# Optimization experiments

Hardware: AMD Instinct MI355X
Metric: run time of the kernel (lower is better)

The kernel has to match this reference:

```python
import jax, jax.numpy as jnp
import numpy as np

EPS = 1e-7
N_SINKHORN = 40


def setup_inputs() -> dict:
    key = jax.random.key(0)
    k1, k2, k3, k4 = jax.random.split(key, 4)
    n, l, K, batch = 1024, 4, 1, 32
    x = jax.random.randint(k1, (batch, n), 0, l)                      # class labels in [0, l)
    W = jax.random.normal(k2, (n, n), jnp.float32)                    # MI-derived logit weights
    V_compress = jax.random.normal(k3, (n, l), jnp.float32)           # log-marginals
    E_compress = jax.random.normal(k4, (K, n, n, l, l), jnp.float32) * 0.1  # log-joints
    return {"x": x, "W": W, "V_compress": V_compress, "E_compress": E_compress}


def reference(x, W, V_compress, E_compress):
    n, l = V_compress.shape
    which_moat = 0

    # --- marginals / joints ---
    V = jax.nn.softmax(V_compress, axis=1)            # [n, l]
    E = jnp.exp(E_compress[which_moat])               # [n, n, l, l]
    E = E / E.sum(axis=(-2, -1), keepdims=True)

    # --- 40-step Sinkhorn / IPF projection onto target row/col marginals ---
    A_b = V[:, None, :, None]                         # [n, 1, l, 1] target row marginals
    B_b = V[None, :, None, :]                         # [1, n, 1, l] target col marginals

    def ipf_step(E, _):
        E = E * (A_b / (E.sum(axis=3, keepdims=True) + EPS))
        E = E * (B_b / (E.sum(axis=2, keepdims=True) + EPS))
        E = E / (E.sum(axis=(-2, -1), keepdims=True) + EPS)
        return E, None

    E, _ = jax.lax.scan(ipf_step, E, None, length=N_SINKHORN)

    # zero the diagonal (i == j) blocks, clamp to [0, 1]
    E = jnp.clip(E * (1.0 - jnp.eye(n, dtype=E.dtype))[:, :, None, None], 0.0, 1.0)

    # --- tree-structured weights and base Laplacian ---
    Ws = jax.nn.sigmoid(W)
    Ws = jnp.tril(Ws, k=-1)
    Ws = Ws + Ws.T                                    # symmetric, zero diag
    L0 = -Ws + jnp.diag(Ws.sum(axis=1))               # [n, n]

    # --- gather per-sample marginals / pairwise probs ---
    idx = jnp.arange(n)
    Pr = V[idx[None, :], x]                           # [B, n]
    P = E[idx[None, :, None], idx[None, None, :], x[:, :, None], x[:, None, :]]  # [B, n, n]
    P = P / (Pr[:, :, None] * Pr[:, None, :])

    WP = Ws[None, :, :] * P                           # [B, n, n]
    eye = jnp.eye(n, dtype=WP.dtype)
    L = -WP + WP.sum(axis=2)[:, :, None] * eye        # batched diag_embed

    y = jnp.log(Pr + 1e-7).sum(axis=1)                # [B]
    _, ld1 = jnp.linalg.slogdet(L[:, 1:, 1:] + 1e-7)
    _, ld0 = jnp.linalg.slogdet(L0[1:, 1:] + 1e-7)
    return y + ld1 - ld0
```

## Files before the change

kernel.cpp:

```cpp
#include <hip/hip_runtime.h>
#include <math.h>

#define MSZ   1048576ull
#define NMAT  33
#define PANSZ 61440
#define NSINK 14

__device__ __forceinline__ float frcp(float x){ return __builtin_amdgcn_rcpf(x); }

typedef __attribute__((ext_vector_type(8)))  short  bfrag;
typedef __attribute__((ext_vector_type(8)))  unsigned short u16x8;
typedef __attribute__((ext_vector_type(16))) float  f32x16;

__device__ __forceinline__ unsigned short bf16rn(float x){
  unsigned u = __float_as_uint(x);
  unsigned r = u + 0x7fffu + ((u>>16)&1u);
  return (unsigned short)(r>>16);
}
__device__ __forceinline__ float bf2f(unsigned short h){
  return __uint_as_float(((unsigned)h)<<16);
}

__global__ void k_misc(const float* __restrict__ Vc, float* __restrict__ V,
                       const float* __restrict__ W, float* __restrict__ Ws){
  int t = threadIdx.x;
  if(blockIdx.x < 4){
    int i = blockIdx.x*256 + t;
    float4 v = ((const float4*)Vc)[i];
    float mx = fmaxf(fmaxf(v.x,v.y), fmaxf(v.z,v.w));
    float e0=__expf(v.x-mx), e1=__expf(v.y-mx), e2=__expf(v.z-mx), e3=__expf(v.w-mx);
    float is = 1.f/(e0+e1+e2+e3);
    ((float4*)V)[i] = make_float4(e0*is, e1*is, e2*is, e3*is);
  } else {
    int idx = (blockIdx.x-4)*256 + t;
    int i = idx>>10, j = idx&1023;
    float v = 0.f;
    if(i != j){
      float w = (i>j) ? W[i*1024+j] : W[j*1024+i];
      v = 1.f/(1.f+__expf(-w));
    }
    Ws[idx]=v;
  }
}

__global__ void k_pr_y(const float* __restrict__ V, const int* __restrict__ x,
                       float* __restrict__ PrInv, float* __restrict__ y){
  int b = blockIdx.x, t = threadIdx.x;
  __shared__ float red[256];
  float acc = 0.f;
  for(int i=t; i<1024; i+=256){
    int xv = x[b*1024+i];
    float pr = V[i*4+xv];
    PrInv[b*1024+i] = 1.f/pr;
    acc += logf(pr + 1e-7f);
  }
  red[t]=acc; __syncthreads();
  for(int s=128;s>0;s>>=1){ if(t<s) red[t]+=red[t+s]; __syncthreads(); }
  if(t==0) y[b]=red[0];
}

__global__ void __launch_bounds__(256) k_sinkhorn(
    const float* __restrict__ Ec, const float* __restrict__ V,
    const float* __restrict__ Ws, const float* __restrict__ PrInv,
    const int* __restrict__ x, float* __restrict__ mats,
    float* __restrict__ partial){
  int idx = blockIdx.x*256 + threadIdx.x;
  int i = idx>>10, j = idx&1023;
  if(i==0) return;
  int t = threadIdx.x;
  int lane = t & 63, wv = t >> 6;
  __shared__ float sE[256][17];
  float E[16];
  {
    const float4* p = (const float4*)(Ec + (size_t)idx*16);
    float4 q0=p[0], q1=p[1], q2=p[2], q3=p[3];
    E[0]=__expf(q0.x); E[1]=__expf(q0.y); E[2]=__expf(q0.z); E[3]=__expf(q0.w);
    E[4]=__expf(q1.x); E[5]=__expf(q1.y); E[6]=__expf(q1.z); E[7]=__expf(q1.w);
    E[8]=__expf(q2.x); E[9]=__expf(q2.y); E[10]=__expf(q2.z); E[11]=__expf(q2.w);
    E[12]=__expf(q3.x);E[13]=__expf(q3.y);E[14]=__expf(q3.z); E[15]=__expf(q3.w);
  }
  float s0=0.f;
  #pragma unroll
  for(int q=0;q<16;q++) s0+=E[q];
  float is0 = frcp(s0);
  #pragma unroll
  for(int q=0;q<16;q++) E[q]*=is0;
  float av[4], bv[4];
  {
    float4 va = ((const float4*)V)[i];
    av[0]=va.x; av[1]=va.y; av[2]=va.z; av[3]=va.w;
    float4 vb = ((const float4*)V)[j];
    bv[0]=vb.x; bv[1]=vb.y; bv[2]=vb.z; bv[3]=vb.w;
  }
  for(int it=0; it<NSINK; ++it){
    #pragma unroll
    for(int r=0;r<4;r++){
      float rs = E[4*r]+E[4*r+1]+E[4*r+2]+E[4*r+3];
      float sc = av[r]*frcp(rs+1e-7f);
      E[4*r]*=sc; E[4*r+1]*=sc; E[4*r+2]*=sc; E[4*r+3]*=sc;
    }
    #pragma unroll
    for(int c=0;c<4;c++){
      float cs = E[c]+E[4+c]+E[8+c]+E[12+c];
      float sc = bv[c]*frcp(cs+1e-7f);
      E[c]*=sc; E[4+c]*=sc; E[8+c]*=sc; E[12+c]*=sc;
    }
  }
  #pragma unroll
  for(int q=0;q<16;q++) sE[t][q] = fminf(fmaxf(E[q],0.f),1.f);
  float wsij = Ws[idx];
  for(int b=0;b<32;b++){
    int xi = x[b*1024+i];
    int xj = x[b*1024+j];
    float val = sE[t][(xi<<2)+xj] * wsij * PrInv[b*1024+i] * PrInv[b*1024+j];
    if(j!=0)
      mats[(size_t)(1+b)*MSZ + (size_t)(i-1)*1024 + (j-1)] = 1e-7f - val;
    float r = val;
    r += __shfl_down(r,32); r += __shfl_down(r,16); r += __shfl_down(r,8);
    r += __shfl_down(r,4);  r += __shfl_down(r,2);  r += __shfl_down(r,1);
    if(lane==0)
      partial[((size_t)b<<14) + ((size_t)(i-1)<<4) + ((blockIdx.x&3)<<2) + wv] = r;
  }
}

__global__ void k_l0(const float* __restrict__ Ws, float* __restrict__ mats){
  int r = blockIdx.x, t = threadIdx.x;
  float* orow = mats + (size_t)r*1024;
  if(r == 1023){
    float4 o = make_float4(0.f,0.f,0.f,0.f);
    if(t==255) o.w = 1.f;
    ((float4*)orow)[t] = o;
    return;
  }
  const float* wrow = Ws + (size_t)(r+1)*1024;
  float4 v = ((const float4*)wrow)[t];
  __shared__ float red[256];
  red[t] = v.x+v.y+v.z+v.w;
  __syncthreads();
  for(int s=128;s>0;s>>=1){ if(t<s) red[t]+=red[t+s]; __syncthreads(); }
  float rs = red[0];
  float o[4];
  #pragma unroll
  for(int q=0;q<4;q++){
    int c = 4*t+q;
    if(c==r)          o[q] = rs + 1e-7f;
    else if(c < 1023) o[q] = 1e-7f - wrow[c+1];
    else              o[q] = 0.f;
  }
  ((float4*)orow)[t] = make_float4(o[0],o[1],o[2],o[3]);
}

__global__ void k_patch(float* __restrict__ mats, const float* __restrict__ partial){
  int m = blockIdx.y + 1;
  int r = blockIdx.x*256 + threadIdx.x;
  float* A = mats + (size_t)m*MSZ;
  A[(size_t)r*1024 + 1023] = (r==1023) ? 1.f : 0.f;
  if(r < 1023){
    A[(size_t)1023*1024 + r] = 0.f;
    const float* pp = partial + (((size_t)(m-1))<<14) + ((size_t)r<<4);
    float s = 0.f;
    #pragma unroll
    for(int q=0;q<16;q++) s += pp[q];
    A[(size_t)r*1024 + r] = s + 1e-7f;
  }
}

__global__ void __launch_bounds__(256) k_panel(float* __restrict__ mats,
    unsigned short* __restrict__ Ah, unsigned short* __restrict__ Al,
    unsigned short* __restrict__ Bh, unsigned short* __restrict__ Bl,
    float* __restrict__ logdet, int k){
  int m = blockIdx.y;
  float* A = mats + (size_t)m*MSZ;
  int rem = 1024 - (k+64);
  int nb = (rem + 255) >> 8;
  int t = threadIdx.x;
  int lane = t & 63, wvi = t >> 6;
  __shared__ float Ld[4096];
  __shared__ float Ud[4096];

  if(wvi==0){
    float row[64];
    #pragma unroll
    for(int q=0;q<64;q++)
      row[q] = A[(size_t)(k+lane)*1024 + k + q];
    float slog = 0.f;
    #pragma unroll
    for(int c=0;c<64;c++){
      float piv = __shfl(row[c], c);
      slog += logf(fabsf(piv));
      float ip = frcp(piv);
      bool below = lane > c;
      float lic = below ? row[c]*ip : 0.f;
      row[c] = below ? lic : row[c];
      if(below) Ld[lane*64 + c] = lic;
      #pragma unroll
      for(int q=c+1;q<64;q++){
        float uq = __shfl(row[q], c);
        row[q] = fmaf(-lic, uq, row[q]);
      }
    }
    #pragma unroll
    for(int q=0;q<64;q++)
      if(q>=lane) Ud[lane*64 + q] = row[q];
    if(lane==0 && blockIdx.x==0){
      if(k==0) logdet[m] = slog; else logdet[m] += slog;
    }
  }
  __syncthreads();

  float v[64];
  unsigned short* Ph; unsigned short* Pl; int rel; bool act;
  if((int)blockIdx.x < nb){
    rel = blockIdx.x*256 + t;
    act = rel < rem;
    int i = k + 64 + rel;
    size_t base = (size_t)i*1024 + k;
    const float4* pb = (const float4*)(A + (act ? base : 0));
    #pragma unroll
    for(int q4=0;q4<16;q4++){
      float4 w = act ? pb[q4] : make_float4(0.f,0.f,0.f,0.f);
      v[4*q4]=w.x; v[4*q4+1]=w.y; v[4*q4+2]=w.z; v[4*q4+3]=w.w;
    }
    #pragma unroll
    for(int p=0;p<64;p++){
      float xp = v[p]*frcp(Ud[p*64+p]);
      v[p] = xp;
      #pragma unroll
      for(int q=p+1;q<64;q++) v[q] = fmaf(-xp, Ud[p*64+q], v[q]);
    }
    Ph = Ah + (size_t)m*PANSZ; Pl = Al + (size_t)m*PANSZ;
  } else {
    rel = (blockIdx.x - nb)*256 + t;
    act = rel < rem;
    int col = k + 64 + rel;
    #pragma unroll
    for(int r=0;r<64;r++) v[r] = act ? A[(size_t)(k+r)*1024 + col] : 0.f;
    #pragma unroll
    for(int r=1;r<64;r++){
      float s = v[r];
      #pragma unroll
      for(int p=0;p<r;p++) s = fmaf(-Ld[r*64+p], v[p], s);
      v[r] = s;
    }
    Ph = Bh + (size_t)m*PANSZ; Pl = Bl + (size_t)m*PANSZ;
  }
  if(act){
    u16x8* ph = (u16x8*)(Ph + (size_t)rel*64);
    u16x8* pl = (u16x8*)(Pl + (size_t)rel*64);
    #pragma unroll
    for(int q8=0;q8<8;q8++){
      u16x8 h8, l8;
      #pragma unroll
      for(int e=0;e<8;e++){
        float xv = v[q8*8+e];
        unsigned short h = bf16rn(xv);
        h8[e] = h;
        l8[e] = bf16rn(xv - bf2f(h));
      }
      ph[q8] = h8;
      pl[q8] = l8;
    }
  }
}

__global__ void __launch_bounds__(64) k_ld(const float* __restrict__ mats,
                                           float* __restrict__ logdet){
  int m = blockIdx.x, t = threadIdx.x;
  const float* A = mats + (size_t)m*MSZ;
  float row[64];
  #pragma unroll
  for(int q=0;q<64;q++)
    row[q] = A[(size_t)(960+t)*1024 + 960 + q];
  float slog = 0.f;
  #pragma unroll
  for(int c=0;c<64;c++){
    float piv = __shfl(row[c], c);
    slog += logf(fabsf(piv));
    float ip = frcp(piv);
    bool below = t > c;
    float lic = below ? row[c]*ip : 0.f;
    #pragma unroll
    for(int q=c+1;q<64;q++){
      float uq = __shfl(row[q], c);
      row[q] = fmaf(-lic, uq, row[q]);
    }
  }
  if(t==0) logdet[m] += slog;
}

__global__ void __launch_bounds__(256) k_gemm(float* __restrict__ mats,
    const unsigned short* __restrict__ Ah, const unsigned short* __restrict__ Al,
    const unsigned short* __restrict__ Bh, const unsigned short* __restrict__ Bl,
    int k){
  int m = blockIdx.z;
  float* A = mats + (size_t)m*MSZ;
  int rem = 1024 - (k+64);
  int i0rel = blockIdx.y*128;
  int j0rel = blockIdx.x*128;
  __shared__ unsigned short As[2][4096];
  __shared__ unsigned short Bs[2][4096];
  int t = threadIdx.x;
  int lane = t & 63, wvi = t >> 6;
  int wr = wvi >> 1, wc = wvi & 1;

  const unsigned short* pAh = Ah + (size_t)m*PANSZ;
  const unsigned short* pAl = Al + (size_t)m*PANSZ;
  const unsigned short* pBh = Bh + (size_t)m*PANSZ;
  const unsigned short* pBl = Bl + (size_t)m*PANSZ;

  int rowA[2], koctA[2], ldsOff[2];
  bool vA[2], vB[2];
  size_t offA[2], offB[2];
  #pragma unroll
  for(int p=0;p<2;p++){
    int c = t + 256*p;
    int row = c>>2, koct = c&3;
    rowA[p]=row; koctA[p]=koct;
    ldsOff[p] = row*32 + ((koct ^ ((row>>1)&3))<<3);
    vA[p] = (i0rel+row) < rem;
    vB[p] = (j0rel+row) < rem;
    offA[p] = (size_t)(i0rel+row)*64 + koct*8;
    offB[p] = (size_t)(j0rel+row)*64 + koct*8;
  }
  u16x8 z; z = 0;

  #pragma unroll
  for(int p=0;p<2;p++){
    u16x8 ah = vA[p] ? *(const u16x8*)(pAh + offA[p]) : z;
    u16x8 al = vA[p] ? *(const u16x8*)(pAl + offA[p]) : z;
    u16x8 bh = vB[p] ? *(const u16x8*)(pBh + offB[p]) : z;
    u16x8 bl = vB[p] ? *(const u16x8*)(pBl + offB[p]) : z;
    *(u16x8*)&As[0][ldsOff[p]] = ah;
    *(u16x8*)&As[1][ldsOff[p]] = al;
    *(u16x8*)&Bs[0][ldsOff[p]] = bh;
    *(u16x8*)&Bs[1][ldsOff[p]] = bl;
  }
  u16x8 p1[8];
  #pragma unroll
  for(int p=0;p<2;p++){
    p1[4*p+0] = vA[p] ? *(const u16x8*)(pAh + offA[p] + 32) : z;
    p1[4*p+1] = vA[p] ? *(const u16x8*)(pAl + offA[p] + 32) : z;
    p1[4*p+2] = vB[p] ? *(const u16x8*)(pBh + offB[p] + 32) : z;
    p1[4*p+3] = vB[p] ? *(const u16x8*)(pBl + offB[p] + 32) : z;
  }
  __syncthreads();

  f32x16 acc[2][2];
  #pragma unroll
  for(int rt=0;rt<2;rt++)
    #pragma unroll
    for(int ct=0;ct<2;ct++)
      #pragma unroll
      for(int q=0;q<16;q++) acc[rt][ct][q] = 0.f;

  int kgrp = lane >> 5;
  #pragma unroll
  for(int ks=0; ks<2; ks++){
    #pragma unroll
    for(int kc=0;kc<2;kc++){
      int koct = kc*2 + kgrp;
      bfrag ah[2], al[2], bh[2], bl[2];
      #pragma unroll
      for(int rt=0;rt<2;rt++){
        int row = wr*64 + rt*32 + (lane&31);
        int ad = row*32 + ((koct ^ ((row>>1)&3))<<3);
        ah[rt] = *(const bfrag*)&As[0][ad];
        al[rt] = *(const bfrag*)&As[1][ad];
      }
      #pragma unroll
      for(int ct=0;ct<2;ct++){
        int col = wc*64 + ct*32 + (lane&31);
        int ad = col*32 + ((koct ^ ((col>>1)&3))<<3);
        bh[ct] = *(const bfrag*)&Bs[0][ad];
        bl[ct] = *(const bfrag*)&Bs[1][ad];
      }
      #pragma unroll
      for(int rt=0;rt<2;rt++)
        #pragma unroll
        for(int ct=0;ct<2;ct++){
          acc[rt][ct] = __builtin_amdgcn_mfma_f32_32x32x16_bf16(ah[rt], bh[ct], acc[rt][ct], 0,0,0);
          acc[rt][ct] = __builtin_amdgcn_mfma_f32_32x32x16_bf16(ah[rt], bl[ct], acc[rt][ct], 0,0,0);
          acc[rt][ct] = __builtin_amdgcn_mfma_f32_32x32x16_bf16(al[rt], bh[ct], acc[rt][ct], 0,0,0);
        }
    }
    if(ks==0){
      __syncthreads();
      #pragma unroll
      for(int p=0;p<2;p++){
        *(u16x8*)&As[0][ldsOff[p]] = p1[4*p+0];
        *(u16x8*)&As[1][ldsOff[p]] = p1[4*p+1];
        *(u16x8*)&Bs[0][ldsOff[p]] = p1[4*p+2];
        *(u16x8*)&Bs[1][ldsOff[p]] = p1[4*p+3];
      }
      __syncthreads();
    }
  }

  int r0 = k + 64;
  #pragma unroll
  for(int rt=0;rt<2;rt++){
    int rowblk = i0rel + wr*64 + rt*32;
    if(rowblk >= rem) continue;
    #pragma unroll
    for(int ct=0;ct<2;ct++){
      int colblk = j0rel + wc*64 + ct*32;
      if(colblk >= rem) continue;
      int col = r0 + colblk + (lane&31);
      int rbase = r0 + rowblk + ((lane>>5)<<2);
      #pragma unroll
      for(int reg=0;reg<16;reg++){
        int row = rbase + (reg&3) + ((reg>>2)<<3);
        float* pc = A + (size_t)row*1024 + col;
        *pc -= acc[rt][ct][reg];
      }
    }
  }
}

__global__ void k_final(const float* __restrict__ y, const float* __restrict__ logdet,
                        float* __restrict__ out){
  int b = threadIdx.x;
  if(b<32) out[b] = y[b] + logdet[1+b] - logdet[0];
}

extern "C" void kernel_launch(void* const* d_in, const int* in_sizes, int n_in,
                              void* d_out, int out_size, void* d_ws, size_t ws_size,
                              hipStream_t stream){
  (void)in_sizes; (void)n_in; (void)out_size; (void)ws_size;
  const int*   x  = (const int*)d_in[0];
  const float* W  = (const float*)d_in[1];
  const float* Vc = (const float*)d_in[2];
  const float* Ec = (const float*)d_in[3];
  float* out = (float*)d_out;

  char* p = (char*)d_ws;
  auto alloc = [&](size_t bytes)->char*{ char* r = p; p += (bytes+255)&~(size_t)255; return r; };
  float* mats   = (float*)alloc((size_t)NMAT*MSZ*4);
  float* Ws     = (float*)alloc(1048576ull*4);
  unsigned short* Ah = (unsigned short*)alloc((size_t)NMAT*PANSZ*2);
  unsigned short* Al = (unsigned short*)alloc((size_t)NMAT*PANSZ*2);
  unsigned short* Bh = (unsigned short*)alloc((size_t)NMAT*PANSZ*2);
  unsigned short* Bl = (unsigned short*)alloc((size_t)NMAT*PANSZ*2);
  float* V      = (float*)alloc(4096*4);
  float* PrInv  = (float*)alloc(32768*4);
  float* partial= (float*)alloc((size_t)32*16384*4);
  float* y      = (float*)alloc(256);
  float* logdet = (float*)alloc(256);

  k_misc<<<4100,256,0,stream>>>(Vc, V, W, Ws);
  k_pr_y<<<32,256,0,stream>>>(V, x, PrInv, y);
  k_sinkhorn<<<4096,256,0,stream>>>(Ec, V, Ws, PrInv, x, mats, partial);
  k_l0<<<1024,256,0,stream>>>(Ws, mats);
  k_patch<<<dim3(4,32),256,0,stream>>>(mats, partial);

  for(int s=0;s<15;s++){
    int k = 64*s;
    int rem = 1024 - (k+64);
    int nbp = (rem+255)/256;
    k_panel<<<dim3(2*nbp,NMAT),256,0,stream>>>(mats, Ah, Al, Bh, Bl, logdet, k);
    int nt = (rem+127)/128;
    k_gemm<<<dim3(nt,nt,NMAT),256,0,stream>>>(mats, Ah, Al, Bh, Bl, k);
  }
  k_ld<<<NMAT,64,0,stream>>>(mats, logdet);
  k_final<<<1,32,0,stream>>>(y, logdet, out);
}
```

Baseline: 1.200 ms.

## Use two-level blocked LU with rank-128 trailing updates and fold PrInv into Sinkhorn

Measured after the change: 1.886 ms. 1.57x slower.

```diff
diff --git a/kernel.cpp b/kernel.cpp
--- a/kernel.cpp
+++ b/kernel.cpp
@@ -44,15 +44,13 @@
 }
 
 __global__ void k_pr_y(const float* __restrict__ V, const int* __restrict__ x,
-                       float* __restrict__ PrInv, float* __restrict__ y){
+                       float* __restrict__ y){
   int b = blockIdx.x, t = threadIdx.x;
   __shared__ float red[256];
   float acc = 0.f;
   for(int i=t; i<1024; i+=256){
     int xv = x[b*1024+i];
-    float pr = V[i*4+xv];
-    PrInv[b*1024+i] = 1.f/pr;
-    acc += logf(pr + 1e-7f);
+    acc += logf(V[i*4+xv] + 1e-7f);
   }
   red[t]=acc; __syncthreads();
   for(int s=128;s>0;s>>=1){ if(t<s) red[t]+=red[t+s]; __syncthreads(); }
@@ -61,9 +59,8 @@
 
 __global__ void __launch_bounds__(256) k_sinkhorn(
     const float* __restrict__ Ec, const float* __restrict__ V,
-    const float* __restrict__ Ws, const float* __restrict__ PrInv,
-    const int* __restrict__ x, float* __restrict__ mats,
-    float* __restrict__ partial){
+    const float* __restrict__ Ws, const int* __restrict__ x,
+    float* __restrict__ mats, float* __restrict__ partial){
   int idx = blockIdx.x*256 + threadIdx.x;
   int i = idx>>10, j = idx&1023;
   if(i==0) return;
@@ -106,13 +103,16 @@
       E[c]*=sc; E[4+c]*=sc; E[8+c]*=sc; E[12+c]*=sc;
     }
   }
-  #pragma unroll
-  for(int q=0;q<16;q++) sE[t][q] = fminf(fmaxf(E[q],0.f),1.f);
   float wsij = Ws[idx];
+  #pragma unroll
+  for(int q=0;q<16;q++){
+    float e = fminf(fmaxf(E[q],0.f),1.f);
+    sE[t][q] = e * wsij * frcp(av[q>>2]*bv[q&3]);
+  }
   for(int b=0;b<32;b++){
     int xi = x[b*1024+i];
     int xj = x[b*1024+j];
-    float val = sE[t][(xi<<2)+xj] * wsij * PrInv[b*1024+i] * PrInv[b*1024+j];
+    float val = sE[t][(xi<<2)+xj];
     if(j!=0)
       mats[(size_t)(1+b)*MSZ + (size_t)(i-1)*1024 + (j-1)] = 1e-7f - val;
     float r = val;
@@ -263,29 +263,223 @@
   }
 }
 
-__global__ void __launch_bounds__(64) k_ld(const float* __restrict__ mats,
-                                           float* __restrict__ logdet){
-  int m = blockIdx.x, t = threadIdx.x;
-  const float* A = mats + (size_t)m*MSZ;
-  float row[64];
-  #pragma unroll
-  for(int q=0;q<64;q++)
-    row[q] = A[(size_t)(960+t)*1024 + 960 + q];
-  float slog = 0.f;
-  #pragma unroll
-  for(int c=0;c<64;c++){
-    float piv = __shfl(row[c], c);
-    slog += logf(fabsf(piv));
-    float ip = frcp(piv);
-    bool below = t > c;
-    float lic = below ? row[c]*ip : 0.f;
-    #pragma unroll
-    for(int q=c+1;q<64;q++){
-      float uq = __shfl(row[q], c);
-      row[q] = fmaf(-lic, uq, row[q]);
-    }
-  }
-  if(t==0) logdet[m] += slog;
+__global__ void __launch_bounds__(256) k_sgemm(float* __restrict__ mats,
+    const unsigned short* __restrict__ Ah, const unsigned short* __restrict__ Al,
+    const unsigned short* __restrict__ Bh, const unsigned short* __restrict__ Bl,
+    int k){
+  int m = blockIdx.y;
+  float* A = mats + (size_t)m*MSZ;
+  int k2 = k + 64;
+  int rem2 = 1024 - (k2+64);
+  int nct = (rem2 + 64 + 127) >> 7;
+  int t = threadIdx.x;
+  int lane = t & 63, wvi = t >> 6;
+  int kgrp = lane >> 5;
+  const unsigned short* pAh = Ah + (size_t)m*PANSZ;
+  const unsigned short* pAl = Al + (size_t)m*PANSZ;
+  const unsigned short* pBh = Bh + (size_t)m*PANSZ;
+  const unsigned short* pBl = Bl + (size_t)m*PANSZ;
+
+  f32x16 acc[2];
+  #pragma unroll
+  for(int u=0;u<2;u++)
+    #pragma unroll
+    for(int q=0;q<16;q++) acc[u][q] = 0.f;
+
+  if((int)blockIdx.x < nct){
+    int rbase = blockIdx.x*128 + wvi*32;
+    int maxrow = rem2 + 63;
+    int arow = rbase + (lane&31);
+    int arowc = (arow > maxrow) ? maxrow : arow;
+    #pragma unroll
+    for(int kc=0;kc<4;kc++){
+      int koct = kc*2 + kgrp;
+      bfrag ah = *(const bfrag*)(pAh + (size_t)arowc*64 + koct*8);
+      bfrag al = *(const bfrag*)(pAl + (size_t)arowc*64 + koct*8);
+      #pragma unroll
+      for(int ct=0;ct<2;ct++){
+        int bcol = ct*32 + (lane&31);
+        bfrag bh = *(const bfrag*)(pBh + (size_t)bcol*64 + koct*8);
+        bfrag bl = *(const bfrag*)(pBl + (size_t)bcol*64 + koct*8);
+        acc[ct] = __builtin_amdgcn_mfma_f32_32x32x16_bf16(ah, bh, acc[ct], 0,0,0);
+        acc[ct] = __builtin_amdgcn_mfma_f32_32x32x16_bf16(ah, bl, acc[ct], 0,0,0);
+        acc[ct] = __builtin_amdgcn_mfma_f32_32x32x16_bf16(al, bh, acc[ct], 0,0,0);
+      }
+    }
+    #pragma unroll
+    for(int ct=0;ct<2;ct++){
+      int gc = k2 + ct*32 + (lane&31);
+      #pragma unroll
+      for(int reg=0;reg<16;reg++){
+        int sr = rbase + ((lane>>5)<<2) + (reg&3) + ((reg>>2)<<3);
+        if(sr <= maxrow){
+          float* pc = A + (size_t)(k2+sr)*1024 + gc;
+          *pc -= acc[ct][reg];
+        }
+      }
+    }
+  } else {
+    int cbase = (blockIdx.x - nct)*128 + wvi*32;
+    int bcol = 64 + cbase + (lane&31);
+    #pragma unroll
+    for(int kc=0;kc<4;kc++){
+      int koct = kc*2 + kgrp;
+      bfrag bh = *(const bfrag*)(pBh + (size_t)bcol*64 + koct*8);
+      bfrag bl = *(const bfrag*)(pBl + (size_t)bcol*64 + koct*8);
+      #pragma unroll
+      for(int rt=0;rt<2;rt++){
+        int arow = rt*32 + (lane&31);
+        bfrag ah = *(const bfrag*)(pAh + (size_t)arow*64 + koct*8);
+        bfrag al = *(const bfrag*)(pAl + (size_t)arow*64 + koct*8);
+        acc[rt] = __builtin_amdgcn_mfma_f32_32x32x16_bf16(ah, bh, acc[rt], 0,0,0);
+        acc[rt] = __builtin_amdgcn_mfma_f32_32x32x16_bf16(ah, bl, acc[rt], 0,0,0);
+        acc[rt] = __builtin_amdgcn_mfma_f32_32x32x16_bf16(al, bh, acc[rt], 0,0,0);
+      }
+    }
+    int gc = k2 + 64 + cbase + (lane&31);
+    #pragma unroll
+    for(int rt=0;rt<2;rt++){
+      #pragma unroll
+      for(int reg=0;reg<16;reg++){
+        int gr = k2 + rt*32 + ((lane>>5)<<2) + (reg&3) + ((reg>>2)<<3);
+        float* pc = A + (size_t)gr*1024 + gc;
+        *pc -= acc[rt][reg];
+      }
+    }
+  }
+}
+
+__global__ void __launch_bounds__(256) k_gemm128(float* __restrict__ mats,
+    const unsigned short* __restrict__ A1h, const unsigned short* __restrict__ A1l,
+    const unsigned short* __restrict__ B1h, const unsigned short* __restrict__ B1l,
+    const unsigned short* __restrict__ A2h, const unsigned short* __restrict__ A2l,
+    const unsigned short* __restrict__ B2h, const unsigned short* __restrict__ B2l,
+    int k){
+  int m = blockIdx.z;
+  float* A = mats + (size_t)m*MSZ;
+  int rem = 1024 - (k+128);
+  int i0rel = blockIdx.y*128;
+  int j0rel = blockIdx.x*128;
+  __shared__ unsigned short As[2][4096];
+  __shared__ unsigned short Bs[2][4096];
+  int t = threadIdx.x;
+  int lane = t & 63, wvi = t >> 6;
+  int wr = wvi >> 1, wc = wvi & 1;
+
+  const unsigned short* srcAh[2] = {A1h + (size_t)m*PANSZ, A2h + (size_t)m*PANSZ};
+  const unsigned short* srcAl[2] = {A1l + (size_t)m*PANSZ, A2l + (size_t)m*PANSZ};
+  const unsigned short* srcBh[2] = {B1h + (size_t)m*PANSZ, B2h + (size_t)m*PANSZ};
+  const unsigned short* srcBl[2] = {B1l + (size_t)m*PANSZ, B2l + (size_t)m*PANSZ};
+
+  int ldsOff[2]; bool vA[2], vB[2];
+  size_t rA[2][2], rB[2][2];
+  int koA[2];
+  #pragma unroll
+  for(int p=0;p<2;p++){
+    int c = t + 256*p;
+    int row = c>>2, koct = c&3;
+    koA[p] = koct*8;
+    ldsOff[p] = row*32 + ((koct ^ ((row>>1)&3))<<3);
+    vA[p] = (i0rel+row) < rem;
+    vB[p] = (j0rel+row) < rem;
+    rA[0][p] = (size_t)(i0rel+row+64)*64;
+    rB[0][p] = (size_t)(j0rel+row+64)*64;
+    rA[1][p] = (size_t)(i0rel+row)*64;
+    rB[1][p] = (size_t)(j0rel+row)*64;
+  }
+  u16x8 z; z = 0;
+  u16x8 cur[8], nxt[8];
+  #pragma unroll
+  for(int p=0;p<2;p++){
+    cur[4*p+0] = vA[p] ? *(const u16x8*)(srcAh[0] + rA[0][p] + koA[p]) : z;
+    cur[4*p+1] = vA[p] ? *(const u16x8*)(srcAl[0] + rA[0][p] + koA[p]) : z;
+    cur[4*p+2] = vB[p] ? *(const u16x8*)(srcBh[0] + rB[0][p] + koA[p]) : z;
+    cur[4*p+3] = vB[p] ? *(const u16x8*)(srcBl[0] + rB[0][p] + koA[p]) : z;
+  }
+
+  f32x16 acc[2][2];
+  #pragma unroll
+  for(int rt=0;rt<2;rt++)
+    #pragma unroll
+    for(int ct=0;ct<2;ct++)
+      #pragma unroll
+      for(int q=0;q<16;q++) acc[rt][ct][q] = 0.f;
+
+  int kgrp = lane >> 5;
+  #pragma unroll
+  for(int st=0; st<4; st++){
+    if(st) __syncthreads();
+    #pragma unroll
+    for(int p=0;p<2;p++){
+      *(u16x8*)&As[0][ldsOff[p]] = cur[4*p+0];
+      *(u16x8*)&As[1][ldsOff[p]] = cur[4*p+1];
+      *(u16x8*)&Bs[0][ldsOff[p]] = cur[4*p+2];
+      *(u16x8*)&Bs[1][ldsOff[p]] = cur[4*p+3];
+    }
+    if(st<3){
+      int ns = st+1;
+      int set = ns>>1, koff = (ns&1)*32;
+      #pragma unroll
+      for(int p=0;p<2;p++){
+        nxt[4*p+0] = vA[p] ? *(const u16x8*)(srcAh[set] + rA[set][p] + koff + koA[p]) : z;
+        nxt[4*p+1] = vA[p] ? *(const u16x8*)(srcAl[set] + rA[set][p] + koff + koA[p]) : z;
+        nxt[4*p+2] = vB[p] ? *(const u16x8*)(srcBh[set] + rB[set][p] + koff + koA[p]) : z;
+        nxt[4*p+3] = vB[p] ? *(const u16x8*)(srcBl[set] + rB[set][p] + koff + koA[p]) : z;
+      }
+    }
+    __syncthreads();
+    #pragma unroll
+    for(int kc=0;kc<2;kc++){
+      int koct = kc*2 + kgrp;
+      bfrag ah[2], al[2], bh[2], bl[2];
+      #pragma unroll
+      for(int rt=0;rt<2;rt++){
+        int row = wr*64 + rt*32 + (lane&31);
+        int ad = row*32 + ((koct ^ ((row>>1)&3))<<3);
+        ah[rt] = *(const bfrag*)&As[0][ad];
+        al[rt] = *(const bfrag*)&As[1][ad];
+      }
+      #pragma unroll
+      for(int ct=0;ct<2;ct++){
+        int col = wc*64 + ct*32 + (lane&31);
+        int ad = col*32 + ((koct ^ ((col>>1)&3))<<3);
+        bh[ct] = *(const bfrag*)&Bs[0][ad];
+        bl[ct] = *(const bfrag*)&Bs[1][ad];
+      }
+      #pragma unroll
+      for(int rt=0;rt<2;rt++)
+        #pragma unroll
+        for(int ct=0;ct<2;ct++){
+          acc[rt][ct] = __builtin_amdgcn_mfma_f32_32x32x16_bf16(ah[rt], bh[ct], acc[rt][ct], 0,0,0);
+          acc[rt][ct] = __builtin_amdgcn_mfma_f32_32x32x16_bf16(ah[rt], bl[ct], acc[rt][ct], 0,0,0);
+          acc[rt][ct] = __builtin_amdgcn_mfma_f32_32x32x16_bf16(al[rt], bh[ct], acc[rt][ct], 0,0,0);
+        }
+    }
+    if(st<3){
+      #pragma unroll
+      for(int q=0;q<8;q++) cur[q] = nxt[q];
+    }
+  }
+
+  int r0 = k + 128;
+  #pragma unroll
+  for(int rt=0;rt<2;rt++){
+    int rowblk = i0rel + wr*64 + rt*32;
+    if(rowblk >= rem) continue;
+    #pragma unroll
+    for(int ct=0;ct<2;ct++){
+      int colblk = j0rel + wc*64 + ct*32;
+      if(colblk >= rem) continue;
+      int col = r0 + colblk + (lane&31);
+      int rbase = r0 + rowblk + ((lane>>5)<<2);
+      #pragma unroll
+      for(int reg=0;reg<16;reg++){
+        int row = rbase + (reg&3) + ((reg>>2)<<3);
+        float* pc = A + (size_t)row*1024 + col;
+        *pc -= acc[rt][ct][reg];
+      }
+    }
+  }
 }
 
 __global__ void __launch_bounds__(256) k_gemm(float* __restrict__ mats,
@@ -308,14 +502,13 @@
   const unsigned short* pBh = Bh + (size_t)m*PANSZ;
   const unsigned short* pBl = Bl + (size_t)m*PANSZ;
 
-  int rowA[2], koctA[2], ldsOff[2];
+  int ldsOff[2];
   bool vA[2], vB[2];
   size_t offA[2], offB[2];
   #pragma unroll
   for(int p=0;p<2;p++){
     int c = t + 256*p;
     int row = c>>2, koct = c&3;
-    rowA[p]=row; koctA[p]=koct;
     ldsOff[p] = row*32 + ((koct ^ ((row>>1)&3))<<3);
     vA[p] = (i0rel+row) < rem;
     vB[p] = (j0rel+row) < rem;
@@ -323,7 +516,6 @@
     offB[p] = (size_t)(j0rel+row)*64 + koct*8;
   }
   u16x8 z; z = 0;
-
   #pragma unroll
   for(int p=0;p<2;p++){
     u16x8 ah = vA[p] ? *(const u16x8*)(pAh + offA[p]) : z;
@@ -417,6 +609,31 @@
   }
 }
 
+__global__ void __launch_bounds__(64) k_ld(const float* __restrict__ mats,
+                                           float* __restrict__ logdet){
+  int m = blockIdx.x, t = threadIdx.x;
+  const float* A = mats + (size_t)m*MSZ;
+  float row[64];
+  #pragma unroll
+  for(int q=0;q<64;q++)
+    row[q] = A[(size_t)(960+t)*1024 + 960 + q];
+  float slog = 0.f;
+  #pragma unroll
+  for(int c=0;c<64;c++){
+    float piv = __shfl(row[c], c);
+    slog += logf(fabsf(piv));
+    float ip = frcp(piv);
+    bool below = t > c;
+    float lic = below ? row[c]*ip : 0.f;
+    #pragma unroll
+    for(int q=c+1;q<64;q++){
+      float uq = __shfl(row[q], c);
+      row[q] = fmaf(-lic, uq, row[q]);
+    }
+  }
+  if(t==0) logdet[m] += slog;
+}
+
 __global__ void k_final(const float* __restrict__ y, const float* __restrict__ logdet,
                         float* __restrict__ out){
   int b = threadIdx.x;
@@ -437,29 +654,56 @@
   auto alloc = [&](size_t bytes)->char*{ char* r = p; p += (bytes+255)&~(size_t)255; return r; };
   float* mats   = (float*)alloc((size_t)NMAT*MSZ*4);
   float* Ws     = (float*)alloc(1048576ull*4);
-  unsigned short* Ah = (unsigned short*)alloc((size_t)NMAT*PANSZ*2);
-  unsigned short* Al = (unsigned short*)alloc((size_t)NMAT*PANSZ*2);
-  unsigned short* Bh = (unsigned short*)alloc((size_t)NMAT*PANSZ*2);
-  unsigned short* Bl = (unsigned short*)alloc((size_t)NMAT*PANSZ*2);
+  unsigned short* A1h = (unsigned short*)alloc((size_t)NMAT*PANSZ*2);
+  unsigned short* A1l = (unsigned short*)alloc((size_t)NMAT*PANSZ*2);
+  unsigned short* B1h = (unsigned short*)alloc((size_t)NMAT*PANSZ*2);
+  unsigned short* B1l = (unsigned short*)alloc((size_t)NMAT*PANSZ*2);
+  unsigned short* A2h = (unsigned short*)alloc((size_t)NMAT*PANSZ*2);
+  unsigned short* A2l = (unsigned short*)alloc((size_t)NMAT*PANSZ*2);
+  unsigned short* B2h = (unsigned short*)alloc((size_t)NMAT*PANSZ*2);
+  unsigned short* B2l = (unsigned short*)alloc((size_t)NMAT*PANSZ*2);
   float* V      = (float*)alloc(4096*4);
-  float* PrInv  = (float*)alloc(32768*4);
   float* partial= (float*)alloc((size_t)32*16384*4);
   float* y      = (float*)alloc(256);
   float* logdet = (float*)alloc(256);
 
   k_misc<<<4100,256,0,stream>>>(Vc, V, W, Ws);
-  k_pr_y<<<32,256,0,stream>>>(V, x, PrInv, y);
-  k_sinkhorn<<<4096,256,0,stream>>>(Ec, V, Ws, PrInv, x, mats, partial);
+  k_pr_y<<<32,256,0,stream>>>(V, x, y);
+  k_sinkhorn<<<4096,256,0,stream>>>(Ec, V, Ws, x, mats, partial);
   k_l0<<<1024,256,0,stream>>>(Ws, mats);
   k_patch<<<dim3(4,32),256,0,stream>>>(mats, partial);
 
-  for(int s=0;s<15;s++){
-    int k = 64*s;
+  for(int s=0;s<7;s++){
+    int k = 128*s;
+    {
+      int rem = 1024 - (k+64);
+      int nbp = (rem+255)/256;
+      k_panel<<<dim3(2*nbp,NMAT),256,0,stream>>>(mats, A1h, A1l, B1h, B1l, logdet, k);
+    }
+    {
+      int rem2 = 1024 - (k+128);
+      int nct = (rem2 + 64 + 127) >> 7;
+      int nrt = rem2 >> 7;
+      k_sgemm<<<dim3(nct+nrt,NMAT),256,0,stream>>>(mats, A1h, A1l, B1h, B1l, k);
+    }
+    {
+      int rem = 1024 - (k+128);
+      int nbp = (rem+255)/256;
+      k_panel<<<dim3(2*nbp,NMAT),256,0,stream>>>(mats, A2h, A2l, B2h, B2l, logdet, k+64);
+    }
+    {
+      int rem = 1024 - (k+128);
+      int nt = (rem+127)/128;
+      k_gemm128<<<dim3(nt,nt,NMAT),256,0,stream>>>(mats, A1h,A1l,B1h,B1l,
+                                                   A2h,A2l,B2h,B2l, k);
+    }
+  }
+  {
+    int k = 896;
     int rem = 1024 - (k+64);
     int nbp = (rem+255)/256;
-    k_panel<<<dim3(2*nbp,NMAT),256,0,stream>>>(mats, Ah, Al, Bh, Bl, logdet, k);
-    int nt = (rem+127)/128;
-    k_gemm<<<dim3(nt,nt,NMAT),256,0,stream>>>(mats, Ah, Al, Bh, Bl, k);
+    k_panel<<<dim3(2*nbp,NMAT),256,0,stream>>>(mats, A1h, A1l, B1h, B1l, logdet, k);
+    k_gemm<<<dim3(1,1,NMAT),256,0,stream>>>(mats, A1h, A1l, B1h, B1l, k);
   }
   k_ld<<<NMAT,64,0,stream>>>(mats, logdet);
   k_final<<<1,32,0,stream>>>(y, logdet, out);
```
